# Performance work log

Measured on AMD Instinct MI355X. Metric: run time of the kernel, lower is better.

## Reference

```python
import jax, jax.numpy as jnp
import numpy as np

DIM = 1024
HEADS = 16
HEAD_DIM = DIM // HEADS


def apply_rope(x):
    # x: (B, S, H, D)
    B, S, H, D = x.shape
    half = D // 2
    freqs = 1.0 / (10000.0 ** (jnp.arange(half, dtype=jnp.float32) / half))
    pos = jnp.arange(S, dtype=jnp.float32)
    angles = pos[:, None] * freqs[None, :]          # (S, half)
    sin = jnp.sin(angles)[None, :, None, :]
    cos = jnp.cos(angles)[None, :, None, :]
    x1, x2 = x[..., :half], x[..., half:]
    return jnp.concatenate([x1 * cos - x2 * sin, x1 * sin + x2 * cos], axis=-1)


def setup_inputs() -> dict:
    key = jax.random.key(0)
    ks = jax.random.split(key, 5)
    x = jax.random.normal(ks[0], (2, 2048, DIM), dtype=jnp.float32)
    s = 1.0 / np.sqrt(DIM)
    qkv_w = jax.random.uniform(ks[1], (3 * DIM, DIM), minval=-s, maxval=s, dtype=jnp.float32)
    qkv_b = jax.random.uniform(ks[2], (3 * DIM,), minval=-s, maxval=s, dtype=jnp.float32)
    proj_w = jax.random.uniform(ks[3], (DIM, DIM), minval=-s, maxval=s, dtype=jnp.float32)
    proj_b = jax.random.uniform(ks[4], (DIM,), minval=-s, maxval=s, dtype=jnp.float32)
    return {"x": x, "qkv_w": qkv_w, "qkv_b": qkv_b, "proj_w": proj_w, "proj_b": proj_b}


def reference(x, qkv_w, qkv_b, proj_w, proj_b):
    B, S, D = x.shape
    qkv = x @ qkv_w.T + qkv_b                       # (B, S, 3D)
    q, k, v = jnp.split(qkv, 3, axis=-1)
    q = q.reshape(B, S, HEADS, HEAD_DIM)
    k = k.reshape(B, S, HEADS, HEAD_DIM)
    v = v.reshape(B, S, HEADS, HEAD_DIM)
    q = apply_rope(q)
    k = apply_rope(k)
    scale = 1.0 / np.sqrt(HEAD_DIM)
    attn = jnp.einsum('bqhd,bkhd->bhqk', q, k) * scale
    mask = jnp.triu(jnp.ones((S, S), dtype=bool), k=1)
    attn = jnp.where(mask[None, None], -1e9, attn)
    attn = jax.nn.softmax(attn, axis=-1)
    out = jnp.einsum('bhqk,bkhd->bqhd', attn, v).reshape(B, S, D)
    return out @ proj_w.T + proj_b
```

## Files before the change

kernel.cpp:

```cpp
#include <hip/hip_runtime.h>
#include <hip/hip_bf16.h>
#include <stdint.h>

typedef unsigned short u16;
typedef __attribute__((ext_vector_type(8))) short bf16x8;
typedef __attribute__((ext_vector_type(4))) float f32x4;
typedef __attribute__((ext_vector_type(16))) float f32x16;

typedef __attribute__((address_space(1))) const void gas_t;
typedef __attribute__((address_space(3))) void las_t;

#define DEV __device__ __forceinline__

DEV float bf2f(u16 v){ union{uint32_t u; float f;} x; x.u = ((uint32_t)v)<<16; return x.f; }
DEV u16 f2bf(float f){ union{float f; uint32_t u;} x; x.f=f; uint32_t r = x.u + 0x7fff + ((x.u>>16)&1u); return (u16)(r>>16); }

DEV uint32_t pk2(float a, float b){
  return (uint32_t)f2bf(a) | ((uint32_t)f2bf(b)<<16);
}

DEV uint32_t cvtpk(float a, float b){
  uint32_t r;
  asm("v_cvt_pk_bf16_f32 %0, %1, %2" : "=v"(r) : "v"(a), "v"(b));
  return r;
}

DEV void xswap(uint32_t a, uint32_t b, int hi, uint32_t& ra, uint32_t& rb){
#if __has_builtin(__builtin_amdgcn_permlane32_swap)
  auto r = __builtin_amdgcn_permlane32_swap((int)a, (int)b, false, false);
  ra = (uint32_t)r[0]; rb = (uint32_t)r[1];
#else
  uint32_t sa = (uint32_t)__shfl_xor((int)a, 32);
  uint32_t sb = (uint32_t)__shfl_xor((int)b, 32);
  ra = hi ? sb : a;
  rb = hi ? b  : sa;
#endif
}

DEV void gload_lds16(const u16* g, u16* l){
  __builtin_amdgcn_global_load_lds((gas_t*)g, (las_t*)l, 16, 0, 0);
}

__global__ void cvt_all(const float* __restrict__ s1, u16* __restrict__ d1,
                        const float* __restrict__ s2, u16* __restrict__ d2,
                        const float* __restrict__ s3, u16* __restrict__ d3)
{
  const int n1 = 1048576, n2 = 786432;
  int i = blockIdx.x*256 + threadIdx.x;
  const float* src; u16* dst; int j;
  if(i < n1){ src = s1; dst = d1; j = i; }
  else if(i < n1+n2){ src = s2; dst = d2; j = i - n1; }
  else { src = s3; dst = d3; j = i - n1 - n2; }
  float4 v = ((const float4*)src)[j];
  ushort4 o; o.x=f2bf(v.x); o.y=f2bf(v.y); o.z=f2bf(v.z); o.w=f2bf(v.w);
  ((ushort4*)dst)[j] = o;
}

template<int OUT_F32, int SWZ>
__global__ __launch_bounds__(256,3)
void gemm_bt(const u16* __restrict__ A, const u16* __restrict__ Bw,
             const float* __restrict__ bias, void* __restrict__ Cp, int N)
{
  constexpr int BK = 32, KSTEPS = 1024/BK;
  __shared__ __align__(16) u16 pool[3*8192];
  const int tid = threadIdx.x, w = tid>>6, l = tid&63;
  const int a = l&15, g = l>>4;
  int bx, by;
  if(SWZ){
    const int bid = blockIdx.x;
    const int st = bid >> 6, q = bid & 63;
    bx = (st % 3)*8 + (q & 7);
    by = (st / 3)*8 + (q >> 3);
  } else {
    bx = blockIdx.x; by = blockIdx.y;
  }
  const int m0 = by*128, n0 = bx*128;
  const int wr = w>>1, wc = w&1;
  f32x4 zero = {0.f,0.f,0.f,0.f};
  f32x4 acc[4][4];
  #pragma unroll
  for(int m=0;m<4;m++) for(int n=0;n<4;n++) acc[m][n]=zero;

  const int srow = l>>2, scol = (l&3)*8;
  const u16* Ag = A  + (size_t)(m0 + w*32 + srow)*1024 + scol;
  const u16* Bg = Bw + (size_t)(n0 + w*32 + srow)*1024 + scol;

#define STAGE(KIDX, BUF) {                                        \
    u16* ab = pool + (BUF)*8192 + w*1024;                         \
    u16* bb = pool + (BUF)*8192 + 4096 + w*1024;                  \
    gload_lds16(Ag + (KIDX)*BK,           ab);                    \
    gload_lds16(Ag + (KIDX)*BK + 16*1024, ab + 512);              \
    gload_lds16(Bg + (KIDX)*BK,           bb);                    \
    gload_lds16(Bg + (KIDX)*BK + 16*1024, bb + 512);              \
  }

  STAGE(0, 0);
  STAGE(1, 1);

  int bc = 0, bn = 2;
  for(int kt=0; kt<KSTEPS; ++kt){
    if(kt+1 < KSTEPS) asm volatile("s_waitcnt vmcnt(4)" ::: "memory");
    else              asm volatile("s_waitcnt vmcnt(0)" ::: "memory");
    __builtin_amdgcn_s_barrier();
    __builtin_amdgcn_sched_barrier(0);

    if(kt+2 < KSTEPS) STAGE(kt+2, bn);

    const u16* AsB = pool + bc*8192;
    const u16* BsB = AsB + 4096;
    bf16x8 af[4], bf[4];
    #pragma unroll
    for(int m=0;m<4;m++) af[m] = *(const bf16x8*)(AsB + (wr*64 + m*16 + a)*BK + g*8);
    #pragma unroll
    for(int n=0;n<4;n++) bf[n] = *(const bf16x8*)(BsB + (wc*64 + n*16 + a)*BK + g*8);
    #pragma unroll
    for(int m=0;m<4;m++)
      #pragma unroll
      for(int n=0;n<4;n++)
        acc[m][n] = __builtin_amdgcn_mfma_f32_16x16x32_bf16(af[m], bf[n], acc[m][n], 0,0,0);

    bc = (bc==2) ? 0 : bc+1;
    bn = (bn==2) ? 0 : bn+1;
  }
#undef STAGE

  if(OUT_F32){
    #pragma unroll
    for(int n=0;n<4;n++){
      int col = n0 + wc*64 + n*16 + a;
      float bv = bias[col];
      #pragma unroll
      for(int m=0;m<4;m++){
        int row = m0 + wr*64 + m*16 + g*4;
        #pragma unroll
        for(int r=0;r<4;r++)
          ((float*)Cp)[(size_t)(row+r)*N + col] = acc[m][n][r] + bv;
      }
    }
  } else {
    __syncthreads();
    u16* cw = pool + (size_t)w*4608;
    #pragma unroll
    for(int n=0;n<4;n++){
      float bv = bias[n0 + wc*64 + n*16 + a];
      #pragma unroll
      for(int m=0;m<4;m++)
        #pragma unroll
        for(int r=0;r<4;r++)
          cw[(m*16 + g*4 + r)*72 + n*16 + a] = f2bf(acc[m][n][r] + bv);
    }
    u16* Cb = (u16*)Cp + (size_t)(m0 + wr*64)*N + n0 + wc*64;
    #pragma unroll
    for(int rr=0;rr<8;rr++){
      int row = rr*8 + (l>>3);
      uint4 v = *(const uint4*)(cw + row*72 + (l&7)*8);
      *(uint4*)(Cb + (size_t)row*N + (l&7)*8) = v;
    }
  }
}

__global__ __launch_bounds__(256,2)
void rope_vt(const u16* __restrict__ qkv, u16* __restrict__ q_r,
             u16* __restrict__ k_r, u16* __restrict__ vt)
{
  __shared__ uint32_t L[64*65];
  const int tid = threadIdx.x;
  const int bh = blockIdx.x & 31;
  const int stile = blockIdx.x >> 5;
  const int b = bh >> 4, h = bh & 15;
  const int s0 = stile*128;

  const int cg = tid & 7, sr = tid >> 3;
  const u16* vsrc = qkv + (size_t)(b*2048 + s0)*3072 + 2048 + h*64 + cg*8;
  union U4 { uint4 v; u16 e[8]; };
  U4 v0a, v1a, v0b, v1b;
  v0a.v = *(const uint4*)(vsrc + (size_t)(sr*2    )*3072);
  v1a.v = *(const uint4*)(vsrc + (size_t)(sr*2 + 1)*3072);
  v0b.v = *(const uint4*)(vsrc + (size_t)(64 + sr*2    )*3072);
  v1b.v = *(const uint4*)(vsrc + (size_t)(64 + sr*2 + 1)*3072);
  #pragma unroll
  for(int jj=0;jj<8;jj++){
    L[(cg*8+jj)*65 + sr]      = (uint32_t)v0a.e[jj] | ((uint32_t)v1a.e[jj]<<16);
    L[(cg*8+jj)*65 + 32 + sr] = (uint32_t)v0b.e[jj] | ((uint32_t)v1b.e[jj]<<16);
  }
  __syncthreads();
  {
    const int w = tid>>6, ln = tid&63;
    u16* dst = vt + (size_t)bh*64*2048 + s0;
    #pragma unroll
    for(int dd=0;dd<16;dd++){
      int d = w*16 + dd;
      *(uint32_t*)(dst + (size_t)d*2048 + ln*2) = L[d*65 + ln];
    }
  }

  const float QSC = 0.18033688011112042f;
  #pragma unroll
  for(int it=0; it<2; ++it){
    int t2 = it*256 + tid;
    int row = t2>>2, gI = t2&3;
    int s = s0 + row;
    int d0 = gI*8;
    const u16* base = qkv + (size_t)(b*2048 + s)*3072 + h*64 + d0;
    union U { uint4 v; u16 e[8]; };
    U q1,q2,k1,k2, oq1,oq2,ok1,ok2;
    q1.v = *(const uint4*)(base);
    q2.v = *(const uint4*)(base+32);
    k1.v = *(const uint4*)(base+1024);
    k2.v = *(const uint4*)(base+1024+32);
    #pragma unroll
    for(int j=0;j<8;j++){
      float d = (float)(d0+j);
      float fr = __expf(-0.28782313662425574f * d);
      float ang = (float)s * fr;
      float sn, cs; sincosf(ang, &sn, &cs);
      float snq = sn*QSC, csq = cs*QSC;
      float x1 = bf2f(q1.e[j]), x2 = bf2f(q2.e[j]);
      oq1.e[j] = f2bf(x1*csq - x2*snq); oq2.e[j] = f2bf(x1*snq + x2*csq);
      x1 = bf2f(k1.e[j]); x2 = bf2f(k2.e[j]);
      ok1.e[j] = f2bf(x1*cs - x2*sn); ok2.e[j] = f2bf(x1*sn + x2*cs);
    }
    size_t o = ((size_t)bh*2048 + s)*64 + d0;
    *(uint4*)(q_r+o) = oq1.v; *(uint4*)(q_r+o+32) = oq2.v;
    *(uint4*)(k_r+o) = ok1.v; *(uint4*)(k_r+o+32) = ok2.v;
  }
}

__global__ __launch_bounds__(256,4)
void attn_fwd8(const u16* __restrict__ Q, const u16* __restrict__ K,
               const u16* __restrict__ VT, u16* __restrict__ O)
{
  __shared__ __align__(16) u16 Ks[2][64][64];
  __shared__ __align__(16) u16 Vs[2][64][64];
  const int tid = threadIdx.x, w = tid>>6, ln = tid&63;
  const int lo = ln&31, hi = ln>>5;
  const int wq = w>>1, wk = w&1;
  const int b0 = blockIdx.x;
  const int bh = b0 & 31;
  const int j64 = 31 - (b0 >> 5);
  const int q0 = j64*64 + wq*32;
  const int nt = j64 + 1;

  const u16* Qb = Q  + ((size_t)bh*2048 + q0)*64;
  const u16* Kb = K  + (size_t)bh*2048*64;
  const u16* Vt = VT + (size_t)bh*64*2048;

  bf16x8 qf[4];
  #pragma unroll
  for(int s=0;s<4;s++) qf[s] = *(const bf16x8*)(Qb + lo*64 + s*16 + hi*8);

  const int rsub = ln>>3;
  const int coloff = ((ln&7) ^ rsub) * 8;
  const int wrow = (w&1)*32;
  const size_t rstride = (w<2) ? 64 : 2048;
  const u16* src0 = (w<2) ? (Kb + (size_t)(wrow+rsub)*64 + coloff)
                          : (Vt + (size_t)(wrow+rsub)*2048 + coloff);
  u16* ldsw = (w<2) ? (&Ks[0][0][0] + wrow*64) : (&Vs[0][0][0] + wrow*64);

  f32x16 oacc0, oacc1, z16;
  #pragma unroll
  for(int r=0;r<16;r++){ oacc0[r]=0.f; oacc1[r]=0.f; z16[r]=0.f; }
  float l_loc = 0.f;
  const int swz = (lo&7)<<4;

  #pragma unroll
  for(int g=0;g<4;g++) gload_lds16(src0 + (size_t)g*8*rstride, ldsw + g*512);
  __syncthreads();

  int buf = 0;
  for(int t=0; t<nt; ++t){
    if(t+1 < nt){
      const size_t koff = (w<2) ? (size_t)(t+1)*64*64 : (size_t)(t+1)*64;
      u16* dst = ldsw + (buf^1)*4096;
      #pragma unroll
      for(int g=0;g<4;g++) gload_lds16(src0 + koff + (size_t)g*8*rstride, dst + g*512);
    }

    const int kv32 = t*64 + wk*32;
    if(kv32 <= q0 + 31){
      const u16* KsB = &Ks[buf][0][0];
      const u16* VsB = &Vs[buf][0][0];
      bf16x8 kf[4], vf[4];
      #pragma unroll
      for(int s=0;s<4;s++)
        kf[s] = *(const bf16x8*)(KsB + (wk*32+lo)*64 + (((s*32 + hi*16) ^ swz)>>1));
      #pragma unroll
      for(int dt=0;dt<2;dt++)
        #pragma unroll
        for(int s2=0;s2<2;s2++)
          vf[dt*2+s2] = *(const bf16x8*)(VsB + (dt*32+lo)*64 + (((wk*64 + s2*32 + hi*16) ^ swz)>>1));

      __builtin_amdgcn_s_setprio(1);
      f32x16 st = __builtin_amdgcn_mfma_f32_32x32x16_bf16(kf[0], qf[0], z16, 0,0,0);
      #pragma unroll
      for(int s=1;s<4;s++)
        st = __builtin_amdgcn_mfma_f32_32x32x16_bf16(kf[s], qf[s], st, 0,0,0);
      __builtin_amdgcn_s_setprio(0);

      float p[16];
      #pragma unroll
      for(int r=0;r<16;r++) p[r] = exp2f(st[r]);
      if(kv32 == q0){
        #pragma unroll
        for(int r=0;r<16;r++){
          const int kvg = (r&3) + 8*(r>>2) + 4*hi;
          p[r] = (kvg <= lo) ? p[r] : 0.f;
        }
      }

      float sm[8];
      #pragma unroll
      for(int i=0;i<8;i++) sm[i] = p[i] + p[i+8];
      #pragma unroll
      for(int s=4;s>=1;s>>=1)
        #pragma unroll
        for(int i=0;i<s;i++) sm[i] += sm[i+s];
      l_loc += sm[0];

      uint32_t pk[8];
      #pragma unroll
      for(int i=0;i<8;i++) pk[i] = cvtpk(p[2*i], p[2*i+1]);

      union PF { bf16x8 v; uint32_t u[4]; } pf0, pf1;
      xswap(pk[0], pk[2], hi, pf0.u[0], pf0.u[2]);
      xswap(pk[1], pk[3], hi, pf0.u[1], pf0.u[3]);
      xswap(pk[4], pk[6], hi, pf1.u[0], pf1.u[2]);
      xswap(pk[5], pk[7], hi, pf1.u[1], pf1.u[3]);

      __builtin_amdgcn_s_setprio(1);
      oacc0 = __builtin_amdgcn_mfma_f32_32x32x16_bf16(vf[0], pf0.v, oacc0, 0,0,0);
      oacc0 = __builtin_amdgcn_mfma_f32_32x32x16_bf16(vf[1], pf1.v, oacc0, 0,0,0);
      oacc1 = __builtin_amdgcn_mfma_f32_32x32x16_bf16(vf[2], pf0.v, oacc1, 0,0,0);
      oacc1 = __builtin_amdgcn_mfma_f32_32x32x16_bf16(vf[3], pf1.v, oacc1, 0,0,0);
      __builtin_amdgcn_s_setprio(0);
    }
    __syncthreads();
    buf ^= 1;
  }

  float l_run = l_loc + __shfl_xor(l_loc, 32);

  float* LoC = (float*)&Ks[0][0][0];
  float* LlC = (float*)&Vs[0][0][0];
  if(wk == 1){
    #pragma unroll
    for(int r=0;r<16;r++){
      const int d = 4*hi + (r&3) + 8*(r>>2);
      LoC[(wq*64 + d   )*32 + lo] = oacc0[r];
      LoC[(wq*64 + d+32)*32 + lo] = oacc1[r];
    }
    if(hi==0) LlC[wq*32 + lo] = l_run;
  }
  __syncthreads();
  if(wk == 0){
    l_run += LlC[wq*32 + lo];
    #pragma unroll
    for(int r=0;r<16;r++){
      const int d = 4*hi + (r&3) + 8*(r>>2);
      oacc0[r] += LoC[(wq*64 + d   )*32 + lo];
      oacc1[r] += LoC[(wq*64 + d+32)*32 + lo];
    }
    const float invl = 1.f / l_run;
    const int row_g = (bh>>4)*2048 + q0 + lo;
    u16* Ob = O + (size_t)row_g*1024 + (bh&15)*64;
    #pragma unroll
    for(int g2=0; g2<4; g2++){
      uint2 pr;
      pr.x = pk2(oacc0[4*g2+0]*invl, oacc0[4*g2+1]*invl);
      pr.y = pk2(oacc0[4*g2+2]*invl, oacc0[4*g2+3]*invl);
      *(uint2*)(Ob + 8*g2 + 4*hi) = pr;
    }
    #pragma unroll
    for(int g2=0; g2<4; g2++){
      uint2 pr;
      pr.x = pk2(oacc1[4*g2+0]*invl, oacc1[4*g2+1]*invl);
      pr.y = pk2(oacc1[4*g2+2]*invl, oacc1[4*g2+3]*invl);
      *(uint2*)(Ob + 32 + 8*g2 + 4*hi) = pr;
    }
  }
}

extern "C" void kernel_launch(void* const* d_in, const int* in_sizes, int n_in,
                              void* d_out, int out_size, void* d_ws, size_t ws_size,
                              hipStream_t stream)
{
  const float* x      = (const float*)d_in[0];
  const float* qkv_w  = (const float*)d_in[1];
  const float* qkv_b  = (const float*)d_in[2];
  const float* proj_w = (const float*)d_in[3];
  const float* proj_b = (const float*)d_in[4];
  float* out = (float*)d_out;
  char* ws = (char*)d_ws;

  u16* xb    = (u16*)(ws);
  u16* wqkv  = (u16*)(ws + 8388608);
  u16* wproj = (u16*)(ws + 8388608 + 6291456);
  u16* qkvr  = (u16*)(ws + 16777216);
  u16* q_r   = (u16*)(ws + 41943040);
  u16* k_r   = q_r + 4194304;
  u16* vt    = k_r + 4194304;
  u16* o_b   = xb;

  cvt_all<<<8192,256,0,stream>>>(x, xb, qkv_w, wqkv, proj_w, wproj);

  gemm_bt<0,1><<<768,256,0,stream>>>(xb, wqkv, qkv_b, qkvr, 3072);

  rope_vt<<<512,256,0,stream>>>(qkvr, q_r, k_r, vt);

  attn_fwd8<<<1024,256,0,stream>>>(q_r, k_r, vt, o_b);

  dim3 gC(8,32);
  gemm_bt<1,0><<<gC,256,0,stream>>>(o_b, wproj, proj_b, out, 1024);
}
```

Measured before the change: 106.0 us.

## Split attention into 32-row query blocks with four-way KV split across waves

The attention kernel now gives each block a single 32-row query tile and has its four waves each take a different 32-key slice of a 128-key stage, then reduces the four partial outputs through LDS. The grid doubles to 2048 blocks, which improves load balance over the causal triangle and wastes less work on the diagonal. In exchange it drops the double-buffered prefetch, so global loads are followed directly by a barrier and are no longer overlapped with compute. The final cross-wave reduction also costs more.

```diff
diff --git a/kernel.cpp b/kernel.cpp
--- a/kernel.cpp
+++ b/kernel.cpp
@@ -227,68 +227,63 @@
 }
 
 __global__ __launch_bounds__(256,4)
-void attn_fwd8(const u16* __restrict__ Q, const u16* __restrict__ K,
-               const u16* __restrict__ VT, u16* __restrict__ O)
+void attn_fwd11(const u16* __restrict__ Q, const u16* __restrict__ K,
+                const u16* __restrict__ VT, u16* __restrict__ O)
 {
-  __shared__ __align__(16) u16 Ks[2][64][64];
-  __shared__ __align__(16) u16 Vs[2][64][64];
+  __shared__ __align__(16) u16 pool[16384];
+  __shared__ float Ll[3][32];
   const int tid = threadIdx.x, w = tid>>6, ln = tid&63;
   const int lo = ln&31, hi = ln>>5;
-  const int wq = w>>1, wk = w&1;
   const int b0 = blockIdx.x;
   const int bh = b0 & 31;
-  const int j64 = 31 - (b0 >> 5);
-  const int q0 = j64*64 + wq*32;
-  const int nt = j64 + 1;
+  const int j  = 63 - (b0 >> 5);
+  const int q0 = j*32;
+  const int nst = (j + 4) >> 2;
 
   const u16* Qb = Q  + ((size_t)bh*2048 + q0)*64;
-  const u16* Kb = K  + (size_t)bh*2048*64;
-  const u16* Vt = VT + (size_t)bh*64*2048;
+  const u16* Kg = K  + (size_t)bh*2048*64;
+  const u16* Vg = VT + (size_t)bh*64*2048;
 
   bf16x8 qf[4];
   #pragma unroll
   for(int s=0;s<4;s++) qf[s] = *(const bf16x8*)(Qb + lo*64 + s*16 + hi*8);
 
-  const int rsub = ln>>3;
-  const int coloff = ((ln&7) ^ rsub) * 8;
-  const int wrow = (w&1)*32;
-  const size_t rstride = (w<2) ? 64 : 2048;
-  const u16* src0 = (w<2) ? (Kb + (size_t)(wrow+rsub)*64 + coloff)
-                          : (Vt + (size_t)(wrow+rsub)*2048 + coloff);
-  u16* ldsw = (w<2) ? (&Ks[0][0][0] + wrow*64) : (&Vs[0][0][0] + wrow*64);
+  const u16* srcK = Kg + (size_t)(w*32 + (ln>>3))*64 + ((ln&7)^(ln>>3))*8;
+  u16* dstK = pool + (w*32)*64;
 
   f32x16 oacc0, oacc1, z16;
   #pragma unroll
   for(int r=0;r<16;r++){ oacc0[r]=0.f; oacc1[r]=0.f; z16[r]=0.f; }
   float l_loc = 0.f;
-  const int swz = (lo&7)<<4;
-
-  #pragma unroll
-  for(int g=0;g<4;g++) gload_lds16(src0 + (size_t)g*8*rstride, ldsw + g*512);
-  __syncthreads();
-
-  int buf = 0;
-  for(int t=0; t<nt; ++t){
-    if(t+1 < nt){
-      const size_t koff = (w<2) ? (size_t)(t+1)*64*64 : (size_t)(t+1)*64;
-      u16* dst = ldsw + (buf^1)*4096;
-      #pragma unroll
-      for(int g=0;g<4;g++) gload_lds16(src0 + koff + (size_t)g*8*rstride, dst + g*512);
-    }
-
-    const int kv32 = t*64 + wk*32;
-    if(kv32 <= q0 + 31){
-      const u16* KsB = &Ks[buf][0][0];
-      const u16* VsB = &Vs[buf][0][0];
+  const int swz = lo&7;
+
+  for(int t=0; t<nst; ++t){
+    const int kv0 = t*128;
+    #pragma unroll
+    for(int i=0;i<4;i++)
+      gload_lds16(srcK + (size_t)(kv0 + i*8)*64, dstK + i*8*64);
+    #pragma unroll
+    for(int i=0;i<4;i++){
+      const int d = w*16 + i*4 + (ln>>4);
+      const int sc = (ln&15) ^ (d&7);
+      gload_lds16(Vg + (size_t)d*2048 + kv0 + sc*8,
+                  pool + 8192 + (w*16 + i*4)*128);
+    }
+    __syncthreads();
+
+    const int kva = kv0 + w*32;
+    if(kva <= q0 + 31){
+      const u16* Kl = pool;
+      const u16* Vl = pool + 8192;
       bf16x8 kf[4], vf[4];
       #pragma unroll
       for(int s=0;s<4;s++)
-        kf[s] = *(const bf16x8*)(KsB + (wk*32+lo)*64 + (((s*32 + hi*16) ^ swz)>>1));
+        kf[s] = *(const bf16x8*)(Kl + (w*32+lo)*64 + (((s*2+hi) ^ swz)<<3));
       #pragma unroll
       for(int dt=0;dt<2;dt++)
         #pragma unroll
         for(int s2=0;s2<2;s2++)
-          vf[dt*2+s2] = *(const bf16x8*)(VsB + (dt*32+lo)*64 + (((wk*64 + s2*32 + hi*16) ^ swz)>>1));
+          vf[dt*2+s2] = *(const bf16x8*)(Vl + (dt*32+lo)*128 + (((w*4+s2*2+hi) ^ swz)<<3));
 
       __builtin_amdgcn_s_setprio(1);
       f32x16 st = __builtin_amdgcn_mfma_f32_32x32x16_bf16(kf[0], qf[0], z16, 0,0,0);
@@ -300,7 +295,7 @@
       float p[16];
       #pragma unroll
       for(int r=0;r<16;r++) p[r] = exp2f(st[r]);
-      if(kv32 == q0){
+      if(kva == q0){
         #pragma unroll
         for(int r=0;r<16;r++){
           const int kvg = (r&3) + 8*(r>>2) + 4*hi;
@@ -335,30 +330,29 @@
       __builtin_amdgcn_s_setprio(0);
     }
     __syncthreads();
-    buf ^= 1;
   }
 
   float l_run = l_loc + __shfl_xor(l_loc, 32);
 
-  float* LoC = (float*)&Ks[0][0][0];
-  float* LlC = (float*)&Vs[0][0][0];
-  if(wk == 1){
+  float* PF = (float*)pool;
+  if(w >= 1){
+    const int slot = w-1;
     #pragma unroll
     for(int r=0;r<16;r++){
       const int d = 4*hi + (r&3) + 8*(r>>2);
-      LoC[(wq*64 + d   )*32 + lo] = oacc0[r];
-      LoC[(wq*64 + d+32)*32 + lo] = oacc1[r];
-    }
-    if(hi==0) LlC[wq*32 + lo] = l_run;
+      PF[slot*2048 + d*32 + lo]      = oacc0[r];
+      PF[slot*2048 + (d+32)*32 + lo] = oacc1[r];
+    }
+    if(hi == 0) Ll[slot][lo] = l_run;
   }
   __syncthreads();
-  if(wk == 0){
-    l_run += LlC[wq*32 + lo];
+  if(w == 0){
+    l_run += Ll[0][lo] + Ll[1][lo] + Ll[2][lo];
     #pragma unroll
     for(int r=0;r<16;r++){
       const int d = 4*hi + (r&3) + 8*(r>>2);
-      oacc0[r] += LoC[(wq*64 + d   )*32 + lo];
-      oacc1[r] += LoC[(wq*64 + d+32)*32 + lo];
+      oacc0[r] += PF[d*32 + lo]      + PF[2048 + d*32 + lo]      + PF[4096 + d*32 + lo];
+      oacc1[r] += PF[(d+32)*32 + lo] + PF[2048 + (d+32)*32 + lo] + PF[4096 + (d+32)*32 + lo];
     }
     const float invl = 1.f / l_run;
     const int row_g = (bh>>4)*2048 + q0 + lo;
@@ -407,7 +401,7 @@
 
   rope_vt<<<512,256,0,stream>>>(qkvr, q_r, k_r, vt);
 
-  attn_fwd8<<<1024,256,0,stream>>>(q_r, k_r, vt, o_b);
+  attn_fwd11<<<2048,256,0,stream>>>(q_r, k_r, vt, o_b);
 
   dim3 gC(8,32);
   gemm_bt<1,0><<<gC,256,0,stream>>>(o_b, wproj, proj_b, out, 1024);
```

New measurement: 109.6 us. 1.03x slower.

## Add 256x128-tile QKV GEMM with 512 threads and drop attention setprio

Applied to the files above, without the earlier changes.

Replaces the QKV projection GEMM with a new kernel that uses 256x128 output tiles, 512 threads and a triple-buffered direct-to-LDS load pipeline, halving the block count. It also stages the output through LDS so global stores are coalesced. The larger tile is meant to raise operand reuse per loaded K slice and cut redundant global traffic, at the cost of more LDS per block and possibly lower occupancy. Separately, the s_setprio hints around the MFMA sequences in the attention kernel are removed.

```diff
diff --git a/kernel.cpp b/kernel.cpp
--- a/kernel.cpp
+++ b/kernel.cpp
@@ -54,6 +54,87 @@
   float4 v = ((const float4*)src)[j];
   ushort4 o; o.x=f2bf(v.x); o.y=f2bf(v.y); o.z=f2bf(v.z); o.w=f2bf(v.w);
   ((ushort4*)dst)[j] = o;
+}
+
+__global__ __launch_bounds__(512,4)
+void gemm_qkv256(const u16* __restrict__ A, const u16* __restrict__ Bw,
+                 const float* __restrict__ bias, u16* __restrict__ Cp, int N)
+{
+  constexpr int BK = 32, KSTEPS = 1024/BK;
+  __shared__ __align__(16) u16 pool[3*12288];
+  const int tid = threadIdx.x, w = tid>>6, l = tid&63;
+  const int a = l&15, g = l>>4;
+  const int bid = blockIdx.x;
+  const int st = bid >> 6, q = bid & 63;
+  const int bx = (st % 3)*8 + (q & 7);
+  const int by = (st / 3)*8 + (q >> 3);
+  const int m0 = by*256, n0 = bx*128;
+  const int wr = w>>1, wc = w&1;
+  f32x4 zero = {0.f,0.f,0.f,0.f};
+  f32x4 acc[4][4];
+  #pragma unroll
+  for(int m=0;m<4;m++) for(int n=0;n<4;n++) acc[m][n]=zero;
+
+  const int srow = l>>2, scol = (l&3)*8;
+  const u16* Ag = A  + (size_t)(m0 + w*32 + srow)*1024 + scol;
+  const u16* Bg = Bw + (size_t)(n0 + w*16 + srow)*1024 + scol;
+
+#define STAGE(KIDX, BUF) {                                        \
+    u16* ab = pool + (BUF)*12288 + w*1024;                        \
+    u16* bb = pool + (BUF)*12288 + 8192 + w*512;                  \
+    gload_lds16(Ag + (KIDX)*BK,           ab);                    \
+    gload_lds16(Ag + (KIDX)*BK + 16*1024, ab + 512);              \
+    gload_lds16(Bg + (KIDX)*BK,           bb);                    \
+  }
+
+  STAGE(0, 0);
+  STAGE(1, 1);
+
+  int bc = 0, bn = 2;
+  for(int kt=0; kt<KSTEPS; ++kt){
+    if(kt+1 < KSTEPS) asm volatile("s_waitcnt vmcnt(3)" ::: "memory");
+    else              asm volatile("s_waitcnt vmcnt(0)" ::: "memory");
+    __builtin_amdgcn_s_barrier();
+    __builtin_amdgcn_sched_barrier(0);
+
+    if(kt+2 < KSTEPS) STAGE(kt+2, bn);
+
+    const u16* AsB = pool + bc*12288;
+    const u16* BsB = AsB + 8192;
+    bf16x8 af[4], bf[4];
+    #pragma unroll
+    for(int m=0;m<4;m++) af[m] = *(const bf16x8*)(AsB + (wr*64 + m*16 + a)*BK + g*8);
+    #pragma unroll
+    for(int n=0;n<4;n++) bf[n] = *(const bf16x8*)(BsB + (wc*64 + n*16 + a)*BK + g*8);
+    #pragma unroll
+    for(int m=0;m<4;m++)
+      #pragma unroll
+      for(int n=0;n<4;n++)
+        acc[m][n] = __builtin_amdgcn_mfma_f32_16x16x32_bf16(af[m], bf[n], acc[m][n], 0,0,0);
+
+    bc = (bc==2) ? 0 : bc+1;
+    bn = (bn==2) ? 0 : bn+1;
+  }
+#undef STAGE
+
+  __syncthreads();
+  u16* cw = pool + (size_t)w*4608;
+  #pragma unroll
+  for(int n=0;n<4;n++){
+    float bv = bias[n0 + wc*64 + n*16 + a];
+    #pragma unroll
+    for(int m=0;m<4;m++)
+      #pragma unroll
+      for(int r=0;r<4;r++)
+        cw[(m*16 + g*4 + r)*72 + n*16 + a] = f2bf(acc[m][n][r] + bv);
+  }
+  u16* Cb = Cp + (size_t)(m0 + wr*64)*N + n0 + wc*64;
+  #pragma unroll
+  for(int rr=0;rr<8;rr++){
+    int row = rr*8 + (l>>3);
+    uint4 v = *(const uint4*)(cw + row*72 + (l&7)*8);
+    *(uint4*)(Cb + (size_t)row*N + (l&7)*8) = v;
+  }
 }
 
 template<int OUT_F32, int SWZ>
@@ -290,12 +371,10 @@
         for(int s2=0;s2<2;s2++)
           vf[dt*2+s2] = *(const bf16x8*)(VsB + (dt*32+lo)*64 + (((wk*64 + s2*32 + hi*16) ^ swz)>>1));
 
-      __builtin_amdgcn_s_setprio(1);
       f32x16 st = __builtin_amdgcn_mfma_f32_32x32x16_bf16(kf[0], qf[0], z16, 0,0,0);
       #pragma unroll
       for(int s=1;s<4;s++)
         st = __builtin_amdgcn_mfma_f32_32x32x16_bf16(kf[s], qf[s], st, 0,0,0);
-      __builtin_amdgcn_s_setprio(0);
 
       float p[16];
       #pragma unroll
@@ -327,12 +406,10 @@
       xswap(pk[4], pk[6], hi, pf1.u[0], pf1.u[2]);
       xswap(pk[5], pk[7], hi, pf1.u[1], pf1.u[3]);
 
-      __builtin_amdgcn_s_setprio(1);
       oacc0 = __builtin_amdgcn_mfma_f32_32x32x16_bf16(vf[0], pf0.v, oacc0, 0,0,0);
       oacc0 = __builtin_amdgcn_mfma_f32_32x32x16_bf16(vf[1], pf1.v, oacc0, 0,0,0);
       oacc1 = __builtin_amdgcn_mfma_f32_32x32x16_bf16(vf[2], pf0.v, oacc1, 0,0,0);
       oacc1 = __builtin_amdgcn_mfma_f32_32x32x16_bf16(vf[3], pf1.v, oacc1, 0,0,0);
-      __builtin_amdgcn_s_setprio(0);
     }
     __syncthreads();
     buf ^= 1;
@@ -403,7 +480,7 @@
 
   cvt_all<<<8192,256,0,stream>>>(x, xb, qkv_w, wqkv, proj_w, wproj);
 
-  gemm_bt<0,1><<<768,256,0,stream>>>(xb, wqkv, qkv_b, qkvr, 3072);
+  gemm_qkv256<<<384,512,0,stream>>>(xb, wqkv, qkv_b, qkvr, 3072);
 
   rope_vt<<<512,256,0,stream>>>(qkvr, q_r, k_r, vt);
 
```

Measured after the change: 104.4 us. About the same (-1.5%).
